# Kernel optimization log

Hardware: AMD Instinct MI355X
Metric: run time of the kernel (lower is better)

Reference implementation:

```python
import jax, jax.numpy as jnp
import numpy as np

N_NODES = 50000
N_EDGES = 600000
K = 4
BN_EPS = 1e-5


def setup_inputs() -> dict:
    key = jax.random.key(0)
    ks = jax.random.split(key, 8)
    x = jax.random.normal(ks[0], (N_NODES, 128), dtype=jnp.float32)
    edge_index = jax.random.randint(ks[1], (2, N_EDGES), 0, N_NODES, dtype=jnp.int64)
    edge_weight = jax.random.uniform(ks[2], (N_EDGES,), dtype=jnp.float32)
    conv_w = jax.random.normal(ks[3], (10, K, 128, 128), dtype=jnp.float32)
    conv_b = jnp.zeros((10, 128), dtype=jnp.float32)
    bn_gamma = jnp.ones((10, 128), dtype=jnp.float32)
    bn_beta = jnp.zeros((10, 128), dtype=jnp.float32)
    lin_w = jax.random.normal(ks[4], (128, 16), dtype=jnp.float32)
    lin_b = jnp.zeros((16,), dtype=jnp.float32)
    return {"x": x, "edge_index": edge_index, "edge_weight": edge_weight,
            "conv_w": conv_w, "conv_b": conv_b, "bn_gamma": bn_gamma,
            "bn_beta": bn_beta, "lin_w": lin_w, "lin_b": lin_b}


def _cheb_norm(edge_index, edge_weight, n_nodes):
    # PyG ChebConv with lambda_max=2, sym normalization:
    # L_hat = 2L/lambda_max - I = -D^{-1/2} A D^{-1/2}, zero diagonal.
    row, col = edge_index[0], edge_index[1]
    w = jnp.where(row == col, 0.0, edge_weight)  # remove_self_loops
    deg = jax.ops.segment_sum(w, row, num_segments=n_nodes)
    dis = jnp.where(deg > 0, jax.lax.rsqrt(jnp.where(deg > 0, deg, 1.0)), 0.0)
    norm = -dis[row] * w * dis[col]
    return norm


def _propagate(h, norm, src, dst, n_nodes):
    # (L_hat h)[i] = sum over edges (src->dst==i) norm_e * h[src_e]
    return jax.ops.segment_sum(norm[:, None] * h[src], dst, num_segments=n_nodes)


def _cheb_conv(h, norm, src, dst, W, b, n_nodes):
    # W: [K, F_in, F_out]; Chebyshev recurrence T0=h, T1=Lh, Tk=2L T_{k-1} - T_{k-2}
    Tx0 = h
    out = Tx0 @ W[0]
    Tx1 = _propagate(Tx0, norm, src, dst, n_nodes)
    out = out + Tx1 @ W[1]
    for k in range(2, W.shape[0]):
        Tx2 = 2.0 * _propagate(Tx1, norm, src, dst, n_nodes) - Tx0
        out = out + Tx2 @ W[k]
        Tx0, Tx1 = Tx1, Tx2
    return out + b


def _batchnorm(h, gamma, beta):
    mean = jnp.mean(h, axis=0)
    var = jnp.mean(jnp.square(h - mean), axis=0)  # biased, as torch BN
    return gamma * (h - mean) * jax.lax.rsqrt(var + BN_EPS) + beta


def reference(x, edge_index, edge_weight, conv_w, conv_b, bn_gamma, bn_beta, lin_w, lin_b):
    n_nodes = x.shape[0]
    src, dst = edge_index[0], edge_index[1]
    norm = _cheb_norm(edge_index, edge_weight, n_nodes)
    h = x
    for i in range(10):
        h = jax.nn.relu(_cheb_conv(h, norm, src, dst, conv_w[i], conv_b[i], n_nodes))
        h = _batchnorm(h, bn_gamma[i], bn_beta[i])
        # dropout: identity (eval mode / deterministic reference)
    return h @ lin_w + lin_b
```

## Files before the change

kernel.cpp:

```cpp
#include <hip/hip_runtime.h>
#include <hip/hip_bf16.h>
#include <cstddef>

#define NN 50000
#define NE 600000
#define FD 128
#define NL 10
#define BN_EPS 1e-5f
#define NBG ((NN + 127) / 128)
#define SCB ((NN + 255) / 256)

typedef _Float16 f16x8 __attribute__((ext_vector_type(8)));
typedef _Float16 f16x2 __attribute__((ext_vector_type(2)));
typedef float f32x4 __attribute__((ext_vector_type(4)));

__global__ void k_detect(const unsigned int* __restrict__ gamma_raw,
                         const unsigned int* __restrict__ idx_raw,
                         int* __restrict__ flags) {
  if (threadIdx.x == 0 && blockIdx.x == 0) {
    flags[0] = (gamma_raw[0] == 0x3F803F80u) ? 1 : 0;
    int i64 = 1;
    for (int i = 1; i < 64; i += 2)
      if (idx_raw[i] != 0u) i64 = 0;
    flags[1] = i64;
  }
}

__device__ __forceinline__ float ld_f(const void* src, int i, int isbf) {
  if (isbf) {
    unsigned int u = ((const unsigned short*)src)[i];
    return __uint_as_float(u << 16);
  }
  return ((const float*)src)[i];
}

__global__ void k_conv_f(const void* __restrict__ src, float* __restrict__ dst,
                         int n, const int* __restrict__ flags) {
  int i = blockIdx.x * 256 + threadIdx.x;
  if (i >= n) return;
  dst[i] = ld_f(src, i, flags[0]);
}

__global__ void k_conv_i(const void* __restrict__ src, int* __restrict__ dst,
                         int n, const int* __restrict__ flags) {
  int i = blockIdx.x * 256 + threadIdx.x;
  if (i >= n) return;
  if (flags[1]) dst[i] = (int)((const long long*)src)[i];
  else          dst[i] = ((const int*)src)[i];
}

__global__ void k_conv_h(const void* __restrict__ src, unsigned int* __restrict__ dst,
                         int n2, const int* __restrict__ flags) {
  int i = blockIdx.x * 256 + threadIdx.x;
  if (i >= n2) return;
  int isbf = flags[0];
  f16x2 p;
  p.x = (_Float16)ld_f(src, i * 2, isbf);
  p.y = (_Float16)ld_f(src, i * 2 + 1, isbf);
  dst[i] = *(unsigned int*)&p;
}

__global__ void k_prepW(const void* __restrict__ src, unsigned short* __restrict__ dst,
                        const int* __restrict__ flags) {
  int tid = blockIdx.x * 256 + threadIdx.x;
  if (tid >= NL * 16 * 4096) return;
  int L = tid >> 16;
  int r16 = tid & 65535;
  int s = r16 >> 12;
  int r = r16 & 4095;
  int n = r >> 5, kk = r & 31;
  int kc = s >> 2, kb = s & 3;
  int srcIdx = ((L * 4 + kc) * FD + (kb * 32 + kk)) * FD + n;
  _Float16 v = (_Float16)ld_f(src, srcIdx, flags[0]);
  dst[tid] = *(unsigned short*)&v;
}

__global__ void k_conv_params(const void* __restrict__ convb, const void* __restrict__ gamma,
                              const void* __restrict__ beta, const void* __restrict__ linw,
                              const void* __restrict__ linb,
                              float* __restrict__ convbf, float* __restrict__ gammaf,
                              float* __restrict__ betaf, float* __restrict__ linwf,
                              float* __restrict__ linbf, float* __restrict__ stid,
                              const int* __restrict__ flags) {
  int i = blockIdx.x * 256 + threadIdx.x;
  int isbf = flags[0];
  if (i < 1280) convbf[i] = ld_f(convb, i, isbf);
  else if (i < 2560) gammaf[i - 1280] = ld_f(gamma, i - 1280, isbf);
  else if (i < 3840) betaf[i - 2560] = ld_f(beta, i - 2560, isbf);
  else if (i < 5888) linwf[i - 3840] = ld_f(linw, i - 3840, isbf);
  else if (i < 5904) linbf[i - 5888] = ld_f(linb, i - 5888, isbf);
  else if (i < 6032) { int f = i - 5904; stid[f] = 1.f; stid[128 + f] = 0.f; }
}

__global__ void k_deg(const int* __restrict__ src, const int* __restrict__ dst,
                      const float* __restrict__ w, float* __restrict__ deg,
                      int* __restrict__ counts, int m) {
  int e = blockIdx.x * 256 + threadIdx.x;
  if (e >= m) return;
  int s = src[e], d = dst[e];
  float ww = (s == d) ? 0.f : w[e];
  atomicAdd(&deg[s], ww);
  atomicAdd(&counts[d], 1);
}

__global__ void k_dis(float* __restrict__ deg, int n) {
  int i = blockIdx.x * 256 + threadIdx.x;
  if (i >= n) return;
  float d = deg[i];
  deg[i] = (d > 0.f) ? rsqrtf(d) : 0.f;
}

__global__ void k_scan1(const int* __restrict__ counts, int* __restrict__ bsum, int n) {
  __shared__ int sd[256];
  int i = blockIdx.x * 256 + threadIdx.x;
  sd[threadIdx.x] = (i < n) ? counts[i] : 0;
  __syncthreads();
  for (int off = 128; off; off >>= 1) {
    if (threadIdx.x < off) sd[threadIdx.x] += sd[threadIdx.x + off];
    __syncthreads();
  }
  if (threadIdx.x == 0) bsum[blockIdx.x] = sd[0];
}

__global__ void k_scan2(const int* __restrict__ bsum, int* __restrict__ boff, int nb) {
  __shared__ int sd[256];
  int t = threadIdx.x;
  int v = (t < nb) ? bsum[t] : 0;
  sd[t] = v;
  __syncthreads();
  for (int off = 1; off < 256; off <<= 1) {
    int x = sd[t];
    int add = (t >= off) ? sd[t - off] : 0;
    __syncthreads();
    sd[t] = x + add;
    __syncthreads();
  }
  if (t < nb) boff[t] = sd[t] - v;
}

__global__ void k_scan3(const int* __restrict__ counts, const int* __restrict__ boff,
                        int* __restrict__ rowptr, int* __restrict__ cursor, int n, int m) {
  __shared__ int sd[256];
  int t = threadIdx.x;
  int i = blockIdx.x * 256 + t;
  int v = (i < n) ? counts[i] : 0;
  sd[t] = v;
  __syncthreads();
  for (int off = 1; off < 256; off <<= 1) {
    int x = sd[t];
    int add = (t >= off) ? sd[t - off] : 0;
    __syncthreads();
    sd[t] = x + add;
    __syncthreads();
  }
  if (i < n) {
    int excl = boff[blockIdx.x] + sd[t] - v;
    rowptr[i] = excl;
    cursor[i] = excl;
  }
  if (i == n - 1) rowptr[n] = m;
}

__global__ void k_fill(const int* __restrict__ src, const int* __restrict__ dst,
                       const float* __restrict__ w, const float* __restrict__ dis,
                       int* __restrict__ cursor, int2* __restrict__ esw, int m) {
  int e = blockIdx.x * 256 + threadIdx.x;
  if (e >= m) return;
  int s = src[e], d = dst[e];
  float ww = (s == d) ? 0.f : w[e];
  float nv = -dis[s] * ww * dis[d];
  int pos = atomicAdd(&cursor[d], 1);
  esw[pos] = make_int2(s, __float_as_int(nv));
}

__global__ void k_rowsum(const int* __restrict__ rowptr, const int2* __restrict__ esw,
                         float* __restrict__ rowsum, int n) {
  int node = blockIdx.x * 256 + threadIdx.x;
  if (node >= n) return;
  int beg = rowptr[node], end = rowptr[node + 1];
  float s = 0.f;
  for (int e = beg; e < end; e++) s += __int_as_float(esw[e].y);
  rowsum[node] = s;
}

template <int MODE>
__global__ __launch_bounds__(256) void k_prop(const uint4* __restrict__ h128,
                                              const uint4* __restrict__ prev128,
                                              const int* __restrict__ rowptr,
                                              const int2* __restrict__ esw,
                                              const float* __restrict__ st,
                                              const float* __restrict__ rowsum,
                                              uint4* __restrict__ out128, int n) {
  int node = blockIdx.x * 16 + (threadIdx.x >> 4);
  int l = threadIdx.x & 15;
  if (node >= n) return;
  int beg = rowptr[node], end = rowptr[node + 1];
  float a[8];
#pragma unroll
  for (int i = 0; i < 8; i++) a[i] = 0.f;
  for (int e = beg; e < end; e += 8) {
    int   s_[8];
    float w_[8];
#pragma unroll
    for (int j = 0; j < 8; j++) {
      int ee = e + j;
      int ec = (ee < end) ? ee : (end - 1);
      int2 m = esw[ec];
      s_[j] = m.x;
      w_[j] = (ee < end) ? __int_as_float(m.y) : 0.f;
    }
    uint4 g[8];
#pragma unroll
    for (int j = 0; j < 8; j++) g[j] = h128[(size_t)s_[j] * 16 + l];
#pragma unroll
    for (int j = 0; j < 8; j++) {
      f16x2 u0 = *(f16x2*)&g[j].x;
      f16x2 u1 = *(f16x2*)&g[j].y;
      f16x2 u2 = *(f16x2*)&g[j].z;
      f16x2 u3 = *(f16x2*)&g[j].w;
      a[0] = fmaf(w_[j], (float)u0.x, a[0]);
      a[1] = fmaf(w_[j], (float)u0.y, a[1]);
      a[2] = fmaf(w_[j], (float)u1.x, a[2]);
      a[3] = fmaf(w_[j], (float)u1.y, a[3]);
      a[4] = fmaf(w_[j], (float)u2.x, a[4]);
      a[5] = fmaf(w_[j], (float)u2.y, a[5]);
      a[6] = fmaf(w_[j], (float)u3.x, a[6]);
      a[7] = fmaf(w_[j], (float)u3.y, a[7]);
    }
  }
  if (MODE == 0) {
    float4 s0 = *(const float4*)&st[l * 8];
    float4 s1 = *(const float4*)&st[l * 8 + 4];
    float4 t0 = *(const float4*)&st[128 + l * 8];
    float4 t1 = *(const float4*)&st[128 + l * 8 + 4];
    float rs = rowsum[node];
    a[0] = s0.x * a[0] + t0.x * rs;  a[1] = s0.y * a[1] + t0.y * rs;
    a[2] = s0.z * a[2] + t0.z * rs;  a[3] = s0.w * a[3] + t0.w * rs;
    a[4] = s1.x * a[4] + t1.x * rs;  a[5] = s1.y * a[5] + t1.y * rs;
    a[6] = s1.z * a[6] + t1.z * rs;  a[7] = s1.w * a[7] + t1.w * rs;
  } else if (MODE == 1) {
    float4 s0 = *(const float4*)&st[l * 8];
    float4 s1 = *(const float4*)&st[l * 8 + 4];
    float4 t0 = *(const float4*)&st[128 + l * 8];
    float4 t1 = *(const float4*)&st[128 + l * 8 + 4];
    uint4 pv = prev128[(size_t)node * 16 + l];
    f16x2 p0 = *(f16x2*)&pv.x, p1 = *(f16x2*)&pv.y, p2 = *(f16x2*)&pv.z, p3 = *(f16x2*)&pv.w;
    a[0] = 2.f * a[0] - (s0.x * (float)p0.x + t0.x);
    a[1] = 2.f * a[1] - (s0.y * (float)p0.y + t0.y);
    a[2] = 2.f * a[2] - (s0.z * (float)p1.x + t0.z);
    a[3] = 2.f * a[3] - (s0.w * (float)p1.y + t0.w);
    a[4] = 2.f * a[4] - (s1.x * (float)p2.x + t1.x);
    a[5] = 2.f * a[5] - (s1.y * (float)p2.y + t1.y);
    a[6] = 2.f * a[6] - (s1.z * (float)p3.x + t1.z);
    a[7] = 2.f * a[7] - (s1.w * (float)p3.y + t1.w);
  } else {
    uint4 pv = prev128[(size_t)node * 16 + l];
    f16x2 p0 = *(f16x2*)&pv.x, p1 = *(f16x2*)&pv.y, p2 = *(f16x2*)&pv.z, p3 = *(f16x2*)&pv.w;
    a[0] = 2.f * a[0] - (float)p0.x;  a[1] = 2.f * a[1] - (float)p0.y;
    a[2] = 2.f * a[2] - (float)p1.x;  a[3] = 2.f * a[3] - (float)p1.y;
    a[4] = 2.f * a[4] - (float)p2.x;  a[5] = 2.f * a[5] - (float)p2.y;
    a[6] = 2.f * a[6] - (float)p3.x;  a[7] = 2.f * a[7] - (float)p3.y;
  }
  f16x2 o0, o1, o2, o3;
  o0.x = (_Float16)a[0]; o0.y = (_Float16)a[1];
  o1.x = (_Float16)a[2]; o1.y = (_Float16)a[3];
  o2.x = (_Float16)a[4]; o2.y = (_Float16)a[5];
  o3.x = (_Float16)a[6]; o3.y = (_Float16)a[7];
  uint4 o;
  o.x = *(unsigned int*)&o0; o.y = *(unsigned int*)&o1;
  o.z = *(unsigned int*)&o2; o.w = *(unsigned int*)&o3;
  out128[(size_t)node * 16 + l] = o;
}

__global__ __launch_bounds__(256) void k_gemm(const unsigned short* __restrict__ T0h,
                                              const unsigned short* __restrict__ T1h,
                                              const unsigned short* __restrict__ T2h,
                                              const unsigned short* __restrict__ T3h,
                                              const unsigned short* __restrict__ Wt,
                                              const float* __restrict__ bias,
                                              const float* __restrict__ st,
                                              unsigned short* __restrict__ outh,
                                              float* __restrict__ partials, int n) {
  __shared__ unsigned short ldsB[2][128 * 40];
  __shared__ float lps[4][128], lqs[4][128];
  int tid = threadIdx.x;
  int wid = tid >> 6, lane = tid & 63;
  int ln = lane & 15, kg = lane >> 4;
  int r0 = blockIdx.x * 128 + wid * 32;

  f32x4 acc[2][8];
#pragma unroll
  for (int rb = 0; rb < 2; rb++)
#pragma unroll
    for (int nb = 0; nb < 8; nb++) acc[rb][nb] = (f32x4){0.f, 0.f, 0.f, 0.f};

  {
    const uint4* g = (const uint4*)(Wt);
    uint4 a = g[tid], b = g[tid + 256];
    *(uint4*)&ldsB[0][(tid >> 2) * 40 + (tid & 3) * 8] = a;
    *(uint4*)&ldsB[0][((tid >> 2) + 64) * 40 + (tid & 3) * 8] = b;
  }
  __syncthreads();

  int rowA0 = r0 + ln;       if (rowA0 >= n) rowA0 = n - 1;
  int rowA1 = r0 + 16 + ln;  if (rowA1 >= n) rowA1 = n - 1;

#pragma unroll
  for (int kc = 0; kc < 4; ++kc) {
    const unsigned short* T = (kc == 0) ? T0h : (kc == 1) ? T1h : (kc == 2) ? T2h : T3h;
#pragma unroll
    for (int kb = 0; kb < 4; ++kb) {
      const int s = kc * 4 + kb;
      const int cur = s & 1;
      uint4 st0, st1;
      if (s < 15) {
        const uint4* g = (const uint4*)(Wt + (s + 1) * 4096);
        st0 = g[tid]; st1 = g[tid + 256];
      }
      f16x8 a0 = *(const f16x8*)(T + (size_t)rowA0 * FD + kb * 32 + kg * 8);
      f16x8 a1 = *(const f16x8*)(T + (size_t)rowA1 * FD + kb * 32 + kg * 8);
      if (kc == 0) {
        const float* sb = st + kb * 32 + kg * 8;
        const float* tb = st + 128 + kb * 32 + kg * 8;
#pragma unroll
        for (int j = 0; j < 8; j++) {
          a0[j] = (_Float16)(sb[j] * (float)a0[j] + tb[j]);
          a1[j] = (_Float16)(sb[j] * (float)a1[j] + tb[j]);
        }
      }
      f16x8 bf[8];
#pragma unroll
      for (int nb = 0; nb < 8; nb++)
        bf[nb] = *(const f16x8*)&ldsB[cur][(nb * 16 + ln) * 40 + kg * 8];
#pragma unroll
      for (int nb = 0; nb < 8; nb++) {
        acc[0][nb] = __builtin_amdgcn_mfma_f32_16x16x32_f16(a0, bf[nb], acc[0][nb], 0, 0, 0);
        acc[1][nb] = __builtin_amdgcn_mfma_f32_16x16x32_f16(a1, bf[nb], acc[1][nb], 0, 0, 0);
      }
      if (s < 15) {
        *(uint4*)&ldsB[cur ^ 1][(tid >> 2) * 40 + (tid & 3) * 8] = st0;
        *(uint4*)&ldsB[cur ^ 1][((tid >> 2) + 64) * 40 + (tid & 3) * 8] = st1;
      }
      __syncthreads();
    }
  }

  float psum[8], psq[8];
#pragma unroll
  for (int nb = 0; nb < 8; nb++) { psum[nb] = 0.f; psq[nb] = 0.f; }
#pragma unroll
  for (int rb = 0; rb < 2; rb++) {
#pragma unroll
    for (int nb = 0; nb < 8; nb++) {
      int col = nb * 16 + ln;
      float bs = bias[col];
#pragma unroll
      for (int r = 0; r < 4; r++) {
        int row = r0 + rb * 16 + kg * 4 + r;
        if (row < n) {
          float v = acc[rb][nb][r] + bs;
          v = fmaxf(v, 0.f);
          _Float16 hv = (_Float16)v;
          outh[(size_t)row * FD + col] = *(unsigned short*)&hv;
          psum[nb] += v;
          psq[nb] += v * v;
        }
      }
    }
  }
#pragma unroll
  for (int nb = 0; nb < 8; nb++) {
    float sv = psum[nb], qv = psq[nb];
    sv += __shfl_xor(sv, 16); sv += __shfl_xor(sv, 32);
    qv += __shfl_xor(qv, 16); qv += __shfl_xor(qv, 32);
    if (kg == 0) { lps[wid][nb * 16 + ln] = sv; lqs[wid][nb * 16 + ln] = qv; }
  }
  __syncthreads();
  if (tid < 128) {
    float sv = lps[0][tid] + lps[1][tid] + lps[2][tid] + lps[3][tid];
    partials[(size_t)blockIdx.x * 256 + tid] = sv;
  } else {
    int c = tid - 128;
    float qv = lqs[0][c] + lqs[1][c] + lqs[2][c] + lqs[3][c];
    partials[(size_t)blockIdx.x * 256 + 128 + c] = qv;
  }
}

__global__ void k_bnred(const float* __restrict__ partials,
                        const float* __restrict__ gamma, const float* __restrict__ beta,
                        float* __restrict__ st, int nblocks, float invN) {
  int f = blockIdx.x;
  float s = 0.f, q = 0.f;
  for (int b = threadIdx.x; b < nblocks; b += 256) {
    s += partials[(size_t)b * 256 + f];
    q += partials[(size_t)b * 256 + 128 + f];
  }
  __shared__ float sd[256], qd[256];
  sd[threadIdx.x] = s; qd[threadIdx.x] = q;
  __syncthreads();
  for (int off = 128; off; off >>= 1) {
    if (threadIdx.x < off) {
      sd[threadIdx.x] += sd[threadIdx.x + off];
      qd[threadIdx.x] += qd[threadIdx.x + off];
    }
    __syncthreads();
  }
  if (threadIdx.x == 0) {
    float mean = sd[0] * invN;
    float var = qd[0] * invN - mean * mean;
    float sc = gamma[f] * rsqrtf(var + BN_EPS);
    st[f] = sc;
    st[128 + f] = beta[f] - mean * sc;
  }
}

__global__ void k_final(const unsigned short* __restrict__ h, const float* __restrict__ w,
                        const float* __restrict__ b, const float* __restrict__ st,
                        void* __restrict__ out, int n, const int* __restrict__ flags) {
  __shared__ float lw[2048];
  __shared__ float ls[128], lt[128];
  for (int i = threadIdx.x; i < 2048; i += 256) lw[i] = w[i];
  if (threadIdx.x < 128) { ls[threadIdx.x] = st[threadIdx.x]; lt[threadIdx.x] = st[128 + threadIdx.x]; }
  __syncthreads();
  int node = blockIdx.x * 256 + threadIdx.x;
  if (node >= n) return;
  float acc[16];
#pragma unroll
  for (int c = 0; c < 16; c++) acc[c] = b[c];
  const f16x8* hr = (const f16x8*)(h + (size_t)node * FD);
#pragma unroll 2
  for (int k8 = 0; k8 < 16; k8++) {
    f16x8 hv = hr[k8];
#pragma unroll
    for (int j = 0; j < 8; j++) {
      int f = k8 * 8 + j;
      float x = ls[f] * (float)hv[j] + lt[f];
#pragma unroll
      for (int c = 0; c < 16; c++) acc[c] = fmaf(x, lw[f * 16 + c], acc[c]);
    }
  }
  int isbf = flags[0];
  for (int c = 0; c < 16; c++) {
    int idx = node * 16 + c;
    if (isbf) ((__hip_bfloat16*)out)[idx] = __float2bfloat16(acc[c]);
    else      ((float*)out)[idx] = acc[c];
  }
}

extern "C" void kernel_launch(void* const* d_in, const int* in_sizes, int n_in,
                              void* d_out, int out_size, void* d_ws, size_t ws_size,
                              hipStream_t stream) {
  char* p = (char*)d_ws;
  auto take = [&](size_t bytes) -> void* {
    void* r = (void*)p;
    p += (bytes + 255) & ~size_t(255);
    return r;
  };
  int*   flags  = (int*)  take(64);
  int*   idx32  = (int*)  take(sizeof(int) * 2 * NE);
  float* ewf    = (float*)take(sizeof(float) * NE);
  unsigned short* wtws = (unsigned short*)take(sizeof(short) * NL * 16 * 4096);
  float* convbf = (float*)take(sizeof(float) * NL * FD);
  float* gammaf = (float*)take(sizeof(float) * NL * FD);
  float* betaf  = (float*)take(sizeof(float) * NL * FD);
  float* linwf  = (float*)take(sizeof(float) * FD * 16);
  float* linbf  = (float*)take(sizeof(float) * 16);
  float* deg    = (float*)take(sizeof(float) * NN);
  float* rowsum = (float*)take(sizeof(float) * NN);
  int*   counts = (int*)  take(sizeof(int) * NN);
  int*   rowptr = (int*)  take(sizeof(int) * (NN + 1));
  int*   cursor = (int*)  take(sizeof(int) * NN);
  int*   bsum   = (int*)  take(sizeof(int) * SCB);
  int*   boff   = (int*)  take(sizeof(int) * SCB);
  int2*  esw    = (int2*) take(sizeof(int2) * NE);
  unsigned int* hbuf = (unsigned int*)take(sizeof(int) * (size_t)NN * 64);
  unsigned int* t1   = (unsigned int*)take(sizeof(int) * (size_t)NN * 64);
  unsigned int* t2   = (unsigned int*)take(sizeof(int) * (size_t)NN * 64);
  unsigned int* t3   = (unsigned int*)take(sizeof(int) * (size_t)NN * 64);
  float* partials = (float*)take(sizeof(float) * (size_t)NBG * 256);
  float* stcur  = (float*)take(sizeof(float) * 256);
  float* stid   = (float*)take(sizeof(float) * 256);

  k_detect<<<1, 64, 0, stream>>>((const unsigned int*)d_in[5], (const unsigned int*)d_in[1], flags);

  k_conv_i<<<(2 * NE + 255) / 256, 256, 0, stream>>>(d_in[1], idx32, 2 * NE, flags);
  k_conv_h<<<(NN * 64 + 255) / 256, 256, 0, stream>>>(d_in[0], hbuf, NN * 64, flags);
  k_conv_f<<<(NE + 255) / 256, 256, 0, stream>>>(d_in[2], ewf, NE, flags);
  k_prepW<<<(NL * 16 * 4096 + 255) / 256, 256, 0, stream>>>(d_in[3], wtws, flags);
  k_conv_params<<<24, 256, 0, stream>>>(d_in[4], d_in[5], d_in[6], d_in[7], d_in[8],
                                        convbf, gammaf, betaf, linwf, linbf, stid, flags);

  hipMemsetAsync(deg, 0, sizeof(float) * NN, stream);
  hipMemsetAsync(counts, 0, sizeof(int) * NN, stream);

  const int* srcI = idx32;
  const int* dstI = idx32 + NE;
  k_deg<<<(NE + 255) / 256, 256, 0, stream>>>(srcI, dstI, ewf, deg, counts, NE);
  k_dis<<<(NN + 255) / 256, 256, 0, stream>>>(deg, NN);
  k_scan1<<<SCB, 256, 0, stream>>>(counts, bsum, NN);
  k_scan2<<<1, 256, 0, stream>>>(bsum, boff, SCB);
  k_scan3<<<SCB, 256, 0, stream>>>(counts, boff, rowptr, cursor, NN, NE);
  k_fill<<<(NE + 255) / 256, 256, 0, stream>>>(srcI, dstI, ewf, deg, cursor, esw, NE);
  k_rowsum<<<(NN + 255) / 256, 256, 0, stream>>>(rowptr, esw, rowsum, NN);

  for (int L = 0; L < NL; ++L) {
    const unsigned short* Wt = wtws + (size_t)L * 16 * 4096;
    const float* stIn = (L == 0) ? stid : stcur;
    k_prop<0><<<(NN + 15) / 16, 256, 0, stream>>>((const uint4*)hbuf, nullptr, rowptr, esw, stIn, rowsum, (uint4*)t1, NN);
    k_prop<1><<<(NN + 15) / 16, 256, 0, stream>>>((const uint4*)t1, (const uint4*)hbuf, rowptr, esw, stIn, nullptr, (uint4*)t2, NN);
    k_prop<2><<<(NN + 15) / 16, 256, 0, stream>>>((const uint4*)t2, (const uint4*)t1, rowptr, esw, nullptr, nullptr, (uint4*)t3, NN);
    k_gemm<<<NBG, 256, 0, stream>>>((const unsigned short*)hbuf, (const unsigned short*)t1,
                                    (const unsigned short*)t2, (const unsigned short*)t3,
                                    Wt, convbf + L * FD, stIn, (unsigned short*)hbuf, partials, NN);
    k_bnred<<<128, 256, 0, stream>>>(partials, gammaf + L * FD, betaf + L * FD, stcur, NBG, 1.0f / NN);
  }

  k_final<<<(NN + 255) / 256, 256, 0, stream>>>((const unsigned short*)hbuf, linwf, linbf, stcur, d_out, NN, flags);
}
```

Baseline: 1.181 ms.

## Fold Chebyshev recurrence into weights, merge prep kernels, atomic BN stats

The Chebyshev terms are rewritten in a monomial basis (T0-T2, T1-3T3, 2T2, 4T3 folded into the weights), so the propagation kernels no longer read the previous term and MODE 1/2 become a plain scaled SpMM. The five input-conversion kernels are merged into one launch, and the two memsets into one that also zeroes per-layer BN stats. BN partials are now accumulated with atomics instead of a separate reduction kernel, leaving a tiny finalize kernel. This removes one feature-matrix read per propagation and several launches, but it uses fp16 powers of L, which may be less accurate, and atomic float sums are nondeterministic.

Measured after the change: 1.172 ms. No clear change (-0.8%).

```diff
diff --git a/kernel.cpp b/kernel.cpp
--- a/kernel.cpp
+++ b/kernel.cpp
@@ -34,62 +34,68 @@
   return ((const float*)src)[i];
 }
 
-__global__ void k_conv_f(const void* __restrict__ src, float* __restrict__ dst,
-                         int n, const int* __restrict__ flags) {
-  int i = blockIdx.x * 256 + threadIdx.x;
-  if (i >= n) return;
-  dst[i] = ld_f(src, i, flags[0]);
-}
-
-__global__ void k_conv_i(const void* __restrict__ src, int* __restrict__ dst,
-                         int n, const int* __restrict__ flags) {
-  int i = blockIdx.x * 256 + threadIdx.x;
-  if (i >= n) return;
-  if (flags[1]) dst[i] = (int)((const long long*)src)[i];
-  else          dst[i] = ((const int*)src)[i];
-}
-
-__global__ void k_conv_h(const void* __restrict__ src, unsigned int* __restrict__ dst,
-                         int n2, const int* __restrict__ flags) {
-  int i = blockIdx.x * 256 + threadIdx.x;
-  if (i >= n2) return;
+#define R_IDX 1200000
+#define R_H   4400000
+#define R_EW  5000000
+#define R_W   5655360
+#define R_P   5661392
+__global__ void k_pre(const void* __restrict__ x, const void* __restrict__ eidx,
+                      const void* __restrict__ ew, const void* __restrict__ convw,
+                      const void* __restrict__ convb, const void* __restrict__ gamma,
+                      const void* __restrict__ beta, const void* __restrict__ linw,
+                      const void* __restrict__ linb,
+                      int* __restrict__ idx32, unsigned int* __restrict__ hbuf,
+                      float* __restrict__ ewf, unsigned short* __restrict__ wt,
+                      float* __restrict__ convbf, float* __restrict__ gammaf,
+                      float* __restrict__ betaf, float* __restrict__ linwf,
+                      float* __restrict__ linbf, float* __restrict__ stid,
+                      const int* __restrict__ flags) {
+  int gid = blockIdx.x * 256 + threadIdx.x;
   int isbf = flags[0];
-  f16x2 p;
-  p.x = (_Float16)ld_f(src, i * 2, isbf);
-  p.y = (_Float16)ld_f(src, i * 2 + 1, isbf);
-  dst[i] = *(unsigned int*)&p;
-}
-
-__global__ void k_prepW(const void* __restrict__ src, unsigned short* __restrict__ dst,
-                        const int* __restrict__ flags) {
-  int tid = blockIdx.x * 256 + threadIdx.x;
-  if (tid >= NL * 16 * 4096) return;
-  int L = tid >> 16;
-  int r16 = tid & 65535;
-  int s = r16 >> 12;
-  int r = r16 & 4095;
-  int n = r >> 5, kk = r & 31;
-  int kc = s >> 2, kb = s & 3;
-  int srcIdx = ((L * 4 + kc) * FD + (kb * 32 + kk)) * FD + n;
-  _Float16 v = (_Float16)ld_f(src, srcIdx, flags[0]);
-  dst[tid] = *(unsigned short*)&v;
-}
-
-__global__ void k_conv_params(const void* __restrict__ convb, const void* __restrict__ gamma,
-                              const void* __restrict__ beta, const void* __restrict__ linw,
-                              const void* __restrict__ linb,
-                              float* __restrict__ convbf, float* __restrict__ gammaf,
-                              float* __restrict__ betaf, float* __restrict__ linwf,
-                              float* __restrict__ linbf, float* __restrict__ stid,
-                              const int* __restrict__ flags) {
-  int i = blockIdx.x * 256 + threadIdx.x;
-  int isbf = flags[0];
-  if (i < 1280) convbf[i] = ld_f(convb, i, isbf);
-  else if (i < 2560) gammaf[i - 1280] = ld_f(gamma, i - 1280, isbf);
-  else if (i < 3840) betaf[i - 2560] = ld_f(beta, i - 2560, isbf);
-  else if (i < 5888) linwf[i - 3840] = ld_f(linw, i - 3840, isbf);
-  else if (i < 5904) linbf[i - 5888] = ld_f(linb, i - 5888, isbf);
-  else if (i < 6032) { int f = i - 5904; stid[f] = 1.f; stid[128 + f] = 0.f; }
+  if (gid < R_IDX) {
+    if (flags[1]) idx32[gid] = (int)((const long long*)eidx)[gid];
+    else          idx32[gid] = ((const int*)eidx)[gid];
+  } else if (gid < R_H) {
+    int i = gid - R_IDX;
+    f16x2 p;
+    p.x = (_Float16)ld_f(x, i * 2, isbf);
+    p.y = (_Float16)ld_f(x, i * 2 + 1, isbf);
+    hbuf[i] = *(unsigned int*)&p;
+  } else if (gid < R_EW) {
+    int i = gid - R_H;
+    ewf[i] = ld_f(ew, i, isbf);
+  } else if (gid < R_W) {
+    int tid = gid - R_EW;
+    int L = tid >> 16;
+    int r16 = tid & 65535;
+    int s = r16 >> 12;
+    int r = r16 & 4095;
+    int n = r >> 5, kk = r & 31;
+    int kc = s >> 2, kb = s & 3;
+    int krow = kb * 32 + kk;
+    int base = (L * 4) * FD * FD;
+    float v;
+    if (kc == 0)
+      v = ld_f(convw, base + (0 * FD + krow) * FD + n, isbf)
+        - ld_f(convw, base + (2 * FD + krow) * FD + n, isbf);
+    else if (kc == 1)
+      v = ld_f(convw, base + (1 * FD + krow) * FD + n, isbf)
+        - 3.f * ld_f(convw, base + (3 * FD + krow) * FD + n, isbf);
+    else if (kc == 2)
+      v = 2.f * ld_f(convw, base + (2 * FD + krow) * FD + n, isbf);
+    else
+      v = 4.f * ld_f(convw, base + (3 * FD + krow) * FD + n, isbf);
+    _Float16 h = (_Float16)v;
+    wt[tid] = *(unsigned short*)&h;
+  } else if (gid < R_P) {
+    int i = gid - R_W;
+    if (i < 1280) convbf[i] = ld_f(convb, i, isbf);
+    else if (i < 2560) gammaf[i - 1280] = ld_f(gamma, i - 1280, isbf);
+    else if (i < 3840) betaf[i - 2560] = ld_f(beta, i - 2560, isbf);
+    else if (i < 5888) linwf[i - 3840] = ld_f(linw, i - 3840, isbf);
+    else if (i < 5904) linbf[i - 5888] = ld_f(linb, i - 5888, isbf);
+    else { int f = i - 5904; stid[f] = 1.f; stid[128 + f] = 0.f; }
+  }
 }
 
 __global__ void k_deg(const int* __restrict__ src, const int* __restrict__ dst,
@@ -185,7 +191,6 @@
 
 template <int MODE>
 __global__ __launch_bounds__(256) void k_prop(const uint4* __restrict__ h128,
-                                              const uint4* __restrict__ prev128,
                                               const int* __restrict__ rowptr,
                                               const int2* __restrict__ esw,
                                               const float* __restrict__ st,
@@ -238,28 +243,6 @@
     a[2] = s0.z * a[2] + t0.z * rs;  a[3] = s0.w * a[3] + t0.w * rs;
     a[4] = s1.x * a[4] + t1.x * rs;  a[5] = s1.y * a[5] + t1.y * rs;
     a[6] = s1.z * a[6] + t1.z * rs;  a[7] = s1.w * a[7] + t1.w * rs;
-  } else if (MODE == 1) {
-    float4 s0 = *(const float4*)&st[l * 8];
-    float4 s1 = *(const float4*)&st[l * 8 + 4];
-    float4 t0 = *(const float4*)&st[128 + l * 8];
-    float4 t1 = *(const float4*)&st[128 + l * 8 + 4];
-    uint4 pv = prev128[(size_t)node * 16 + l];
-    f16x2 p0 = *(f16x2*)&pv.x, p1 = *(f16x2*)&pv.y, p2 = *(f16x2*)&pv.z, p3 = *(f16x2*)&pv.w;
-    a[0] = 2.f * a[0] - (s0.x * (float)p0.x + t0.x);
-    a[1] = 2.f * a[1] - (s0.y * (float)p0.y + t0.y);
-    a[2] = 2.f * a[2] - (s0.z * (float)p1.x + t0.z);
-    a[3] = 2.f * a[3] - (s0.w * (float)p1.y + t0.w);
-    a[4] = 2.f * a[4] - (s1.x * (float)p2.x + t1.x);
-    a[5] = 2.f * a[5] - (s1.y * (float)p2.y + t1.y);
-    a[6] = 2.f * a[6] - (s1.z * (float)p3.x + t1.z);
-    a[7] = 2.f * a[7] - (s1.w * (float)p3.y + t1.w);
-  } else {
-    uint4 pv = prev128[(size_t)node * 16 + l];
-    f16x2 p0 = *(f16x2*)&pv.x, p1 = *(f16x2*)&pv.y, p2 = *(f16x2*)&pv.z, p3 = *(f16x2*)&pv.w;
-    a[0] = 2.f * a[0] - (float)p0.x;  a[1] = 2.f * a[1] - (float)p0.y;
-    a[2] = 2.f * a[2] - (float)p1.x;  a[3] = 2.f * a[3] - (float)p1.y;
-    a[4] = 2.f * a[4] - (float)p2.x;  a[5] = 2.f * a[5] - (float)p2.y;
-    a[6] = 2.f * a[6] - (float)p3.x;  a[7] = 2.f * a[7] - (float)p3.y;
   }
   f16x2 o0, o1, o2, o3;
   o0.x = (_Float16)a[0]; o0.y = (_Float16)a[1];
@@ -280,7 +263,7 @@
                                               const float* __restrict__ bias,
                                               const float* __restrict__ st,
                                               unsigned short* __restrict__ outh,
-                                              float* __restrict__ partials, int n) {
+                                              float* __restrict__ stats, int n) {
   __shared__ unsigned short ldsB[2][128 * 40];
   __shared__ float lps[4][128], lqs[4][128];
   int tid = threadIdx.x;
@@ -378,40 +361,23 @@
   __syncthreads();
   if (tid < 128) {
     float sv = lps[0][tid] + lps[1][tid] + lps[2][tid] + lps[3][tid];
-    partials[(size_t)blockIdx.x * 256 + tid] = sv;
+    atomicAdd(&stats[tid], sv);
   } else {
     int c = tid - 128;
     float qv = lqs[0][c] + lqs[1][c] + lqs[2][c] + lqs[3][c];
-    partials[(size_t)blockIdx.x * 256 + 128 + c] = qv;
-  }
-}
-
-__global__ void k_bnred(const float* __restrict__ partials,
+    atomicAdd(&stats[128 + c], qv);
+  }
+}
+
+__global__ void k_bnfin(const float* __restrict__ stats,
                         const float* __restrict__ gamma, const float* __restrict__ beta,
-                        float* __restrict__ st, int nblocks, float invN) {
-  int f = blockIdx.x;
-  float s = 0.f, q = 0.f;
-  for (int b = threadIdx.x; b < nblocks; b += 256) {
-    s += partials[(size_t)b * 256 + f];
-    q += partials[(size_t)b * 256 + 128 + f];
-  }
-  __shared__ float sd[256], qd[256];
-  sd[threadIdx.x] = s; qd[threadIdx.x] = q;
-  __syncthreads();
-  for (int off = 128; off; off >>= 1) {
-    if (threadIdx.x < off) {
-      sd[threadIdx.x] += sd[threadIdx.x + off];
-      qd[threadIdx.x] += qd[threadIdx.x + off];
-    }
-    __syncthreads();
-  }
-  if (threadIdx.x == 0) {
-    float mean = sd[0] * invN;
-    float var = qd[0] * invN - mean * mean;
-    float sc = gamma[f] * rsqrtf(var + BN_EPS);
-    st[f] = sc;
-    st[128 + f] = beta[f] - mean * sc;
-  }
+                        float* __restrict__ st, float invN) {
+  int f = threadIdx.x;
+  float mean = stats[f] * invN;
+  float var = stats[128 + f] * invN - mean * mean;
+  float sc = gamma[f] * rsqrtf(var + BN_EPS);
+  st[f] = sc;
+  st[128 + f] = beta[f] - mean * sc;
 }
 
 __global__ void k_final(const unsigned short* __restrict__ h, const float* __restrict__ w,
@@ -465,9 +431,11 @@
   float* betaf  = (float*)take(sizeof(float) * NL * FD);
   float* linwf  = (float*)take(sizeof(float) * FD * 16);
   float* linbf  = (float*)take(sizeof(float) * 16);
-  float* deg    = (float*)take(sizeof(float) * NN);
+  char*  zb     = (char*) take(sizeof(float) * NN + sizeof(int) * NN + sizeof(float) * NL * 256);
+  float* deg    = (float*)zb;
+  int*   counts = (int*)  (zb + sizeof(float) * NN);
+  float* stats  = (float*)(zb + sizeof(float) * NN + sizeof(int) * NN);
   float* rowsum = (float*)take(sizeof(float) * NN);
-  int*   counts = (int*)  take(sizeof(int) * NN);
   int*   rowptr = (int*)  take(sizeof(int) * (NN + 1));
   int*   cursor = (int*)  take(sizeof(int) * NN);
   int*   bsum   = (int*)  take(sizeof(int) * SCB);
@@ -477,21 +445,17 @@
   unsigned int* t1   = (unsigned int*)take(sizeof(int) * (size_t)NN * 64);
   unsigned int* t2   = (unsigned int*)take(sizeof(int) * (size_t)NN * 64);
   unsigned int* t3   = (unsigned int*)take(sizeof(int) * (size_t)NN * 64);
-  float* partials = (float*)take(sizeof(float) * (size_t)NBG * 256);
   float* stcur  = (float*)take(sizeof(float) * 256);
   float* stid   = (float*)take(sizeof(float) * 256);
 
   k_detect<<<1, 64, 0, stream>>>((const unsigned int*)d_in[5], (const unsigned int*)d_in[1], flags);
 
-  k_conv_i<<<(2 * NE + 255) / 256, 256, 0, stream>>>(d_in[1], idx32, 2 * NE, flags);
-  k_conv_h<<<(NN * 64 + 255) / 256, 256, 0, stream>>>(d_in[0], hbuf, NN * 64, flags);
-  k_conv_f<<<(NE + 255) / 256, 256, 0, stream>>>(d_in[2], ewf, NE, flags);
-  k_prepW<<<(NL * 16 * 4096 + 255) / 256, 256, 0, stream>>>(d_in[3], wtws, flags);
-  k_conv_params<<<24, 256, 0, stream>>>(d_in[4], d_in[5], d_in[6], d_in[7], d_in[8],
-                                        convbf, gammaf, betaf, linwf, linbf, stid, flags);
-
-  hipMemsetAsync(deg, 0, sizeof(float) * NN, stream);
-  hipMemsetAsync(counts, 0, sizeof(int) * NN, stream);
+  k_pre<<<(R_P + 255) / 256, 256, 0, stream>>>(d_in[0], d_in[1], d_in[2], d_in[3], d_in[4],
+                                               d_in[5], d_in[6], d_in[7], d_in[8],
+                                               idx32, hbuf, ewf, wtws,
+                                               convbf, gammaf, betaf, linwf, linbf, stid, flags);
+
+  hipMemsetAsync(zb, 0, sizeof(float) * NN + sizeof(int) * NN + sizeof(float) * NL * 256, stream);
 
   const int* srcI = idx32;
   const int* dstI = idx32 + NE;
@@ -506,13 +470,13 @@
   for (int L = 0; L < NL; ++L) {
     const unsigned short* Wt = wtws + (size_t)L * 16 * 4096;
     const float* stIn = (L == 0) ? stid : stcur;
-    k_prop<0><<<(NN + 15) / 16, 256, 0, stream>>>((const uint4*)hbuf, nullptr, rowptr, esw, stIn, rowsum, (uint4*)t1, NN);
-    k_prop<1><<<(NN + 15) / 16, 256, 0, stream>>>((const uint4*)t1, (const uint4*)hbuf, rowptr, esw, stIn, nullptr, (uint4*)t2, NN);
-    k_prop<2><<<(NN + 15) / 16, 256, 0, stream>>>((const uint4*)t2, (const uint4*)t1, rowptr, esw, nullptr, nullptr, (uint4*)t3, NN);
+    k_prop<0><<<(NN + 15) / 16, 256, 0, stream>>>((const uint4*)hbuf, rowptr, esw, stIn, rowsum, (uint4*)t1, NN);
+    k_prop<1><<<(NN + 15) / 16, 256, 0, stream>>>((const uint4*)t1, rowptr, esw, nullptr, nullptr, (uint4*)t2, NN);
+    k_prop<1><<<(NN + 15) / 16, 256, 0, stream>>>((const uint4*)t2, rowptr, esw, nullptr, nullptr, (uint4*)t3, NN);
     k_gemm<<<NBG, 256, 0, stream>>>((const unsigned short*)hbuf, (const unsigned short*)t1,
                                     (const unsigned short*)t2, (const unsigned short*)t3,
-                                    Wt, convbf + L * FD, stIn, (unsigned short*)hbuf, partials, NN);
-    k_bnred<<<128, 256, 0, stream>>>(partials, gammaf + L * FD, betaf + L * FD, stcur, NBG, 1.0f / NN);
+                                    Wt, convbf + L * FD, stIn, (unsigned short*)hbuf, stats + L * 256, NN);
+    k_bnfin<<<1, 128, 0, stream>>>(stats + L * 256, gammaf + L * FD, betaf + L * FD, stcur, 1.0f / NN);
   }
 
   k_final<<<(NN + 255) / 256, 256, 0, stream>>>((const unsigned short*)hbuf, linwf, linbf, stcur, d_out, NN, flags);
```
